# Kernel tuning notes

Hardware: AMD Instinct MI355X
Metric: run time of the kernel (lower is better)

## Reference

```python
import jax, jax.numpy as jnp
import numpy as np

B, C, HS, WS = 4, 256, 64, 64
E, NH, TOPK, MLP = 256, 8, 512, 1024
HD = E // NH
CHUNK = 16   # chunk size over random-query subset for L1 cdist
EPS = 1e-5


def setup_inputs() -> dict:
    key = jax.random.key(0)
    ks = jax.random.split(key, 8)
    s = 0.02
    return {
        "query_source": jax.random.normal(ks[0], (B, C, HS, WS), jnp.float32),
        "context": jax.random.normal(ks[1], (B, C, HS, WS), jnp.float32),
        "rand_token_ind": jax.random.randint(ks[2], (B, TOPK), 0, HS * WS),
        "in_proj_w": jax.random.normal(ks[3], (3 * E, E), jnp.float32) * s,
        "in_proj_b": jnp.zeros((3 * E,), jnp.float32),
        "out_proj_w": jax.random.normal(ks[4], (E, E), jnp.float32) * s,
        "out_proj_b": jnp.zeros((E,), jnp.float32),
        "conv1_w": jax.random.normal(ks[5], (MLP, C), jnp.float32) * s,
        "conv1_b": jnp.zeros((MLP,), jnp.float32),
        "bn1_gamma": jnp.ones((MLP,), jnp.float32),
        "bn1_beta": jnp.zeros((MLP,), jnp.float32),
        "bn1_mean": jnp.zeros((MLP,), jnp.float32),
        "bn1_var": jnp.ones((MLP,), jnp.float32),
        "conv2_w": jax.random.normal(ks[6], (C, MLP), jnp.float32) * s,
        "conv2_b": jnp.zeros((C,), jnp.float32),
        "bn2_gamma": jnp.ones((C,), jnp.float32),
        "bn2_beta": jnp.zeros((C,), jnp.float32),
        "bn2_mean": jnp.zeros((C,), jnp.float32),
        "bn2_var": jnp.ones((C,), jnp.float32),
    }


def _min_l1_dist(K, Qs):
    """min over random-query subset of L1 distances. K:[B,Lkv,D], Qs:[B,tk,D] -> [B,Lkv].
    Chunked scan over tk to avoid materializing [B,Lkv,tk,D]."""
    b, tk, d = Qs.shape
    nc = tk // CHUNK
    Qc = Qs.reshape(b, nc, CHUNK, d).transpose(1, 0, 2, 3)  # [nc,B,CHUNK,D]
    init = jnp.full(K.shape[:2], jnp.inf, K.dtype)

    def step(carry, q):
        dist = jnp.abs(K[:, :, None, :] - q[:, None, :, :]).sum(-1)  # [B,Lkv,CHUNK]
        return jnp.minimum(carry, dist.min(-1)), None

    md, _ = jax.lax.scan(step, init, Qc)
    return md


def _forward(query_source, context, rand_token_ind, in_proj_w, in_proj_b,
             out_proj_w, out_proj_b, conv1_w, conv1_b, bn1_gamma, bn1_beta,
             bn1_mean, bn1_var, conv2_w, conv2_b, bn2_gamma, bn2_beta,
             bn2_mean, bn2_var):
    b, c, h, w = query_source.shape
    q_tok = query_source.reshape(b, c, -1).transpose(0, 2, 1)   # [B,Lq,E]
    kv_tok = context.reshape(b, c, -1).transpose(0, 2, 1)       # [B,Lkv,E]

    # --- dist_to_random_Q_selection (top_k < Lkv) ---
    Qs = jnp.take_along_axis(q_tok, rand_token_ind[:, :, None], axis=1)  # [B,tk,E]
    md = _min_l1_dist(kv_tok, Qs)                                        # [B,Lkv]
    idx = jnp.argsort(md, axis=1)[:, :TOPK]                              # smallest, sorted
    k_sel = jnp.take_along_axis(kv_tok, idx[:, :, None], axis=1)         # [B,TOPK,E]
    v_sel = k_sel                                                        # keys==values==context

    # --- nn.MultiheadAttention (eval, batch_first) ---
    wq, wk, wv = in_proj_w[:E], in_proj_w[E:2 * E], in_proj_w[2 * E:]
    bq, bk, bv = in_proj_b[:E], in_proj_b[E:2 * E], in_proj_b[2 * E:]
    q = (q_tok @ wq.T + bq).reshape(b, -1, NH, HD)
    k = (k_sel @ wk.T + bk).reshape(b, TOPK, NH, HD)
    v = (v_sel @ wv.T + bv).reshape(b, TOPK, NH, HD)
    scores = jnp.einsum('bqhd,bkhd->bhqk', q, k) / jnp.sqrt(jnp.float32(HD))
    attn = jax.nn.softmax(scores, axis=-1)
    ctx = jnp.einsum('bhqk,bkhd->bqhd', attn, v).reshape(b, -1, E)
    out = ctx @ out_proj_w.T + out_proj_b                               # [B,Lq,E]
    attn_out = out.transpose(0, 2, 1).reshape(b, c, h, w)

    # --- residual conv MLP (1x1 convs, batchnorm eval) ---
    def conv1x1(x, wgt, bias):
        return jnp.einsum('bchw,oc->bohw', x, wgt) + bias[None, :, None, None]

    def bn(x, g, bt, m, v_):
        inv = g / jnp.sqrt(v_ + EPS)
        return x * inv[None, :, None, None] + (bt - m * inv)[None, :, None, None]

    hdn = jax.nn.relu(bn(conv1x1(attn_out, conv1_w, conv1_b),
                         bn1_gamma, bn1_beta, bn1_mean, bn1_var))
    y = bn(conv1x1(hdn, conv2_w, conv2_b), bn2_gamma, bn2_beta, bn2_mean, bn2_var)
    return attn_out + y


def reference(query_source, context, rand_token_ind, in_proj_w, in_proj_b,
              out_proj_w, out_proj_b, conv1_w, conv1_b, bn1_gamma, bn1_beta,
              bn1_mean, bn1_var, conv2_w, conv2_b, bn2_gamma, bn2_beta,
              bn2_mean, bn2_var):
    return _forward(query_source, context, rand_token_ind, in_proj_w, in_proj_b,
                    out_proj_w, out_proj_b, conv1_w, conv1_b, bn1_gamma, bn1_beta,
                    bn1_mean, bn1_var, conv2_w, conv2_b, bn2_gamma, bn2_beta,
                    bn2_mean, bn2_var)
```

## Files before the change

kernel.cpp:

```cpp
#include <hip/hip_runtime.h>
#include <math.h>

#define B_ 4
#define C_ 256
#define L_ 4096
#define E_ 256
#define NH_ 8
#define HD_ 32
#define TOPK_ 512
#define MLP_ 1024
#define EPS_ 1e-5f

typedef __attribute__((ext_vector_type(4))) float f32x4;
typedef __attribute__((ext_vector_type(8))) short short8;
typedef __attribute__((ext_vector_type(2))) unsigned int u32x2;
typedef __attribute__((ext_vector_type(4))) unsigned int u32x4;

__device__ __forceinline__ unsigned short f2bf(float x) {
  unsigned u = __float_as_uint(x);
  return (unsigned short)((u + 0x7FFFu + ((u >> 16) & 1)) >> 16);
}
__device__ __forceinline__ float bf2f(unsigned short h) { return __uint_as_float((unsigned)h << 16); }

__device__ __forceinline__ float dpp_red16(float s) {
  s += __int_as_float(__builtin_amdgcn_update_dpp(0, __float_as_int(s), 0x121, 0xF, 0xF, false));
  s += __int_as_float(__builtin_amdgcn_update_dpp(0, __float_as_int(s), 0x122, 0xF, 0xF, false));
  s += __int_as_float(__builtin_amdgcn_update_dpp(0, __float_as_int(s), 0x124, 0xF, 0xF, false));
  s += __int_as_float(__builtin_amdgcn_update_dpp(0, __float_as_int(s), 0x128, 0xF, 0xF, false));
  return s;
}

template <int WRITE_BF>
__global__ __launch_bounds__(256) void k_transpose(const float* __restrict__ in, float* __restrict__ out,
                                                   unsigned short* __restrict__ outbf) {
  __shared__ float tile[32][33];
  int b = blockIdx.z;
  int l0 = blockIdx.x * 32, c0 = blockIdx.y * 32;
  const float* ib = in + (long)b * C_ * L_;
  float* ob = out + (long)b * L_ * C_;
  int tx = threadIdx.x, ty = threadIdx.y;
#pragma unroll
  for (int i = ty; i < 32; i += 8) tile[i][tx] = ib[(long)(c0 + i) * L_ + l0 + tx];
  __syncthreads();
#pragma unroll
  for (int i = ty; i < 32; i += 8) {
    float v = tile[tx][i];
    long off = (long)(l0 + i) * C_ + c0 + tx;
    ob[off] = v;
    if (WRITE_BF) outbf[(long)b * L_ * C_ + off] = f2bf(v);
  }
}

__device__ __forceinline__ void conv_bf8(const float* __restrict__ W, unsigned short* __restrict__ D, int blk) {
  int i = (blk * 256 + threadIdx.x) * 8;
  float4 x = *(const float4*)(W + i);
  float4 y = *(const float4*)(W + i + 4);
  u32x4 w;
  w.x = (unsigned)f2bf(x.x) | ((unsigned)f2bf(x.y) << 16);
  w.y = (unsigned)f2bf(x.z) | ((unsigned)f2bf(x.w) << 16);
  w.z = (unsigned)f2bf(y.x) | ((unsigned)f2bf(y.y) << 16);
  w.w = (unsigned)f2bf(y.z) | ((unsigned)f2bf(y.w) << 16);
  *(u32x4*)(D + i) = w;
}

__global__ __launch_bounds__(256) void k_prep(const float* __restrict__ ipw, const float* __restrict__ opw,
                                              const float* __restrict__ c1w, const float* __restrict__ c2w,
                                              unsigned short* __restrict__ wq_bf, unsigned short* __restrict__ wkv_bf,
                                              unsigned short* __restrict__ c1w_bf, unsigned short* __restrict__ c2w_bf,
                                              unsigned short* __restrict__ opw_d, unsigned* __restrict__ md) {
  int bx = blockIdx.x;
  if (bx < 32) {
    conv_bf8(ipw, wq_bf, bx);
  } else if (bx < 96) {
    conv_bf8(ipw + 65536, wkv_bf, bx - 32);
  } else if (bx < 224) {
    conv_bf8(c1w, c1w_bf, bx - 96);
  } else if (bx < 352) {
    conv_bf8(c2w, c2w_bf, bx - 224);
  } else if (bx < 416) {
    int i = ((bx - 352) * 256 + threadIdx.x) * 4;
    int k = i & 255;
    int n = i >> 8;
    float4 x = *(const float4*)(opw + i);
    unsigned short h0 = f2bf(x.x), h1 = f2bf(x.y), h2 = f2bf(x.z), h3 = f2bf(x.w);
    unsigned short l0 = f2bf(x.x - bf2f(h0)), l1 = f2bf(x.y - bf2f(h1));
    unsigned short l2 = f2bf(x.z - bf2f(h2)), l3 = f2bf(x.w - bf2f(h3));
    u32x2 hv, lv;
    hv.x = (unsigned)h0 | ((unsigned)h1 << 16); hv.y = (unsigned)h2 | ((unsigned)h3 << 16);
    lv.x = (unsigned)l0 | ((unsigned)l1 << 16); lv.y = (unsigned)l2 | ((unsigned)l3 << 16);
    unsigned short* dst = opw_d + (long)n * 512 + (k >> 5) * 64 + (k & 31);
    *(u32x2*)dst = hv;
    *(u32x2*)(dst + 32) = lv;
  } else {
    md[(bx - 416) * 256 + threadIdx.x] = 0x7f800000u;
  }
}

__global__ __launch_bounds__(256) void k_gather_f32(const float* __restrict__ src, const int* __restrict__ ind,
                                                    float* __restrict__ dst, int nrows) {
  int gr = blockIdx.x * 4 + (threadIdx.x >> 6);
  int b = gr / nrows, r = gr % nrows;
  int c = (threadIdx.x & 63) * 4;
  int idx = ind[b * nrows + r];
  *(float4*)(dst + ((long)b * nrows + r) * C_ + c) = *(const float4*)(src + ((long)b * L_ + idx) * C_ + c);
}

__global__ __launch_bounds__(256) void k_gather_bf(const float* __restrict__ src, const int* __restrict__ ind,
                                                   unsigned short* __restrict__ dst, int nrows) {
  int gr = blockIdx.x * 4 + (threadIdx.x >> 6);
  int b = gr / nrows, r = gr % nrows;
  int c = (threadIdx.x & 63) * 4;
  int idx = ind[b * nrows + r];
  float4 x = *(const float4*)(src + ((long)b * L_ + idx) * C_ + c);
  u32x2 w;
  w.x = (unsigned)f2bf(x.x) | ((unsigned)f2bf(x.y) << 16);
  w.y = (unsigned)f2bf(x.z) | ((unsigned)f2bf(x.w) << 16);
  *(u32x2*)(dst + ((long)b * nrows + r) * C_ + c) = w;
}

__global__ __launch_bounds__(256) void k_dist(const float* __restrict__ Kt, const float* __restrict__ Qs,
                                              unsigned* __restrict__ mdbits) {
  __shared__ float Kl[16 * 256];
  __shared__ unsigned mdl[64];
  const int b = blockIdx.y, tb = blockIdx.x, qz = blockIdx.z;
  const int tid = threadIdx.x;
  const int cg = tid & 15, qslot = tid >> 4;
  f32x4 Q[4][4];
  {
    const float* qbase = Qs + ((long)b * TOPK_ + qz * 64 + qslot) * C_ + cg * 4;
#pragma unroll
    for (int r = 0; r < 4; r++)
#pragma unroll
      for (int i = 0; i < 4; i++)
        Q[r][i] = *(volatile const f32x4*)(qbase + (long)r * 16 * C_ + i * 64);
  }
  if (tid < 64) mdl[tid] = 0x7f800000u;
  for (int ck = 0; ck < 4; ck++) {
    __syncthreads();
    {
      const float4* src = (const float4*)(Kt + ((long)b * L_ + tb * 64 + ck * 16) * C_);
      float4* dst = (float4*)Kl;
#pragma unroll
      for (int j = 0; j < 4; j++) dst[tid + j * 256] = src[tid + j * 256];
    }
    __syncthreads();
    for (int t = 0; t < 16; t++) {
      const float* kp = &Kl[t * 256 + cg * 4];
      float4 k0 = *(const float4*)kp;
      float4 k1 = *(const float4*)(kp + 64);
      float4 k2 = *(const float4*)(kp + 128);
      float4 k3 = *(const float4*)(kp + 192);
      float d0, d1, d2, d3;
#define DIST_R(r, dst_)                                                                                   \
  dst_ = (((fabsf(k0.x - Q[r][0].x) + fabsf(k0.y - Q[r][0].y)) +                                          \
           (fabsf(k0.z - Q[r][0].z) + fabsf(k0.w - Q[r][0].w))) +                                         \
          ((fabsf(k1.x - Q[r][1].x) + fabsf(k1.y - Q[r][1].y)) +                                          \
           (fabsf(k1.z - Q[r][1].z) + fabsf(k1.w - Q[r][1].w)))) +                                        \
         (((fabsf(k2.x - Q[r][2].x) + fabsf(k2.y - Q[r][2].y)) +                                          \
           (fabsf(k2.z - Q[r][2].z) + fabsf(k2.w - Q[r][2].w))) +                                         \
          ((fabsf(k3.x - Q[r][3].x) + fabsf(k3.y - Q[r][3].y)) +                                          \
           (fabsf(k3.z - Q[r][3].z) + fabsf(k3.w - Q[r][3].w))))
      DIST_R(0, d0);
      DIST_R(1, d1);
      DIST_R(2, d2);
      DIST_R(3, d3);
#undef DIST_R
      d0 = dpp_red16(d0);
      d1 = dpp_red16(d1);
      d2 = dpp_red16(d2);
      d3 = dpp_red16(d3);
      float mn = fminf(fminf(d0, d1), fminf(d2, d3));
      mn = fminf(mn, __int_as_float(__builtin_amdgcn_ds_swizzle(__float_as_int(mn), 0x401F)));
      if ((tid & 31) == 0) atomicMin(&mdl[ck * 16 + t], __float_as_uint(mn));
    }
  }
  __syncthreads();
  if (tid < 64) atomicMin(&mdbits[(long)b * L_ + tb * 64 + tid], mdl[tid]);
}

__global__ __launch_bounds__(1024) void k_sort(const unsigned* __restrict__ mdb, unsigned* __restrict__ idxsel) {
  __shared__ unsigned long long s[4096];
  const int b = blockIdx.x, tid = threadIdx.x;
  for (int i = tid; i < 4096; i += 1024)
    s[i] = (((unsigned long long)mdb[b * L_ + i]) << 32) | (unsigned)i;
  __syncthreads();
  for (int k = 2; k <= 4096; k <<= 1)
    for (int j = k >> 1; j > 0; j >>= 1) {
      for (int i = tid; i < 4096; i += 1024) {
        int ixj = i ^ j;
        if (ixj > i) {
          bool up = ((i & k) == 0);
          unsigned long long a = s[i], c = s[ixj];
          if ((a > c) == up) { s[i] = c; s[ixj] = a; }
        }
      }
      __syncthreads();
    }
  for (int i = tid; i < TOPK_; i += 1024) idxsel[b * TOPK_ + i] = (unsigned)(s[i] & 0xFFFFFFFFu);
}

template <int BN, int MODE>
__global__ __launch_bounds__(256) void k_gemm_s(
    const unsigned short* __restrict__ A, const unsigned short* __restrict__ Bm, int K, int N, float cscale,
    const float* __restrict__ bias, const float* __restrict__ g, const float* __restrict__ be,
    const float* __restrict__ mu, const float* __restrict__ va, const float* __restrict__ Xres,
    float* __restrict__ Cf, unsigned short* __restrict__ Cb, unsigned short* __restrict__ Caux) {
  constexpr int NWN = (BN == 128) ? 2 : 1;
  constexpr int WR = (NWN == 2) ? 64 : 32;
  constexpr int MG = WR / 16, NG = 4;
  __shared__ __align__(16) unsigned short As[128 * 64];
  __shared__ __align__(16) unsigned short Bs[BN * 64];
  const int tid = threadIdx.x;
  const int wid = tid >> 6, lane = tid & 63, lr = lane & 15, lg = lane >> 4;
  const int wm = wid / NWN, wn = wid % NWN;
  const int row0 = wm * WR, col0 = wn * 64;
  char* AsB = (char*)As;
  char* BsB = (char*)Bs;
  f32x4 acc[MG][NG];
#pragma unroll
  for (int m = 0; m < MG; m++)
#pragma unroll
    for (int n = 0; n < NG; n++) acc[m][n] = (f32x4){0.f, 0.f, 0.f, 0.f};

  for (int k0 = 0; k0 < K; k0 += 64) {
    if (k0) __syncthreads();
    {
      int r = tid >> 1, h = tid & 1;
      const unsigned short* p = A + (long)(blockIdx.y * 128 + r) * K + k0 + h * 32;
#pragma unroll
      for (int j = 0; j < 4; j++) {
        u32x4 w = *(const u32x4*)(p + j * 8);
        int c = h * 4 + j;
        *(u32x4*)(AsB + r * 128 + ((c ^ (r & 7)) << 4)) = w;
      }
    }
    if (BN == 128) {
      int r = tid >> 1, h = tid & 1;
      const unsigned short* p = Bm + (long)(blockIdx.x * 128 + r) * K + k0 + h * 32;
#pragma unroll
      for (int j = 0; j < 4; j++) {
        u32x4 w = *(const u32x4*)(p + j * 8);
        int c = h * 4 + j;
        *(u32x4*)(BsB + r * 128 + ((c ^ (r & 7)) << 4)) = w;
      }
    } else {
      int r = tid >> 2, qp = tid & 3;
      const unsigned short* p = Bm + (long)(blockIdx.x * 64 + r) * K + k0 + qp * 16;
#pragma unroll
      for (int j = 0; j < 2; j++) {
        u32x4 w = *(const u32x4*)(p + j * 8);
        int c = qp * 2 + j;
        *(u32x4*)(BsB + r * 128 + ((c ^ (r & 7)) << 4)) = w;
      }
    }
    __syncthreads();
    short8 a0[MG], a1[MG], b0[NG], b1[NG];
#pragma unroll
    for (int m = 0; m < MG; m++) {
      int rr = row0 + m * 16 + lr;
      a0[m] = *(const short8*)(AsB + rr * 128 + (((0 + lg) ^ (rr & 7)) << 4));
      a1[m] = *(const short8*)(AsB + rr * 128 + (((4 + lg) ^ (rr & 7)) << 4));
    }
#pragma unroll
    for (int n = 0; n < NG; n++) {
      int rr = col0 + n * 16 + lr;
      b0[n] = *(const short8*)(BsB + rr * 128 + (((0 + lg) ^ (rr & 7)) << 4));
      b1[n] = *(const short8*)(BsB + rr * 128 + (((4 + lg) ^ (rr & 7)) << 4));
    }
#pragma unroll
    for (int m = 0; m < MG; m++)
#pragma unroll
      for (int n = 0; n < NG; n++)
        acc[m][n] = __builtin_amdgcn_mfma_f32_16x16x32_bf16(a0[m], b0[n], acc[m][n], 0, 0, 0);
#pragma unroll
    for (int m = 0; m < MG; m++)
#pragma unroll
      for (int n = 0; n < NG; n++)
        acc[m][n] = __builtin_amdgcn_mfma_f32_16x16x32_bf16(a1[m], b1[n], acc[m][n], 0, 0, 0);
  }
  const int mbase = blockIdx.y * 128 + row0 + lg * 4;
  const int nbase = blockIdx.x * BN + col0;
#pragma unroll
  for (int n = 0; n < NG; n++) {
    int nn = nbase + n * 16 + lr;
    float bb = bias[nn];
    float inv = 0.f, sh = 0.f;
    if (MODE == 3 || MODE == 5) {
      inv = g[nn] / sqrtf(va[nn] + EPS_);
      sh = be[nn] - mu[nn] * inv;
    }
#pragma unroll
    for (int m = 0; m < MG; m++) {
#pragma unroll
      for (int r = 0; r < 4; r++) {
        int mm = mbase + m * 16 + r;
        float v = acc[m][n][r] + bb;
        if (MODE == 0) {
          Cb[(long)mm * N + nn] = f2bf(v * cscale);
        } else if (MODE == 1) {
          if (nn < 256) {
            Cb[(long)mm * 256 + nn] = f2bf(v);
          } else {
            int bi = mm >> 9, t = mm & 511;
            Caux[((long)bi * 256 + (nn - 256)) * 512 + t] = f2bf(v);
          }
        } else if (MODE == 3) {
          v = v * inv + sh;
          v = fmaxf(v, 0.f);
          Cb[(long)mm * N + nn] = f2bf(v);
        } else if (MODE == 5) {
          v = v * inv + sh + Xres[(long)mm * 256 + nn];
          int bi = mm >> 12, l = mm & 4095;
          Cf[(long)bi * (C_ * L_) + (long)nn * L_ + l] = v;
        }
      }
    }
  }
}

__global__ __launch_bounds__(256) void k_gemm_d(const unsigned short* __restrict__ A,
                                                const unsigned short* __restrict__ Bd, int K,
                                                const float* __restrict__ bias, float* __restrict__ Cf,
                                                unsigned short* __restrict__ Cb) {
  constexpr int MG = 2, NG = 4;
  __shared__ __align__(16) unsigned short As[128 * 64];
  __shared__ __align__(16) unsigned short Bs[64 * 64];
  const int tid = threadIdx.x;
  const int wid = tid >> 6, lane = tid & 63, lr = lane & 15, lg = lane >> 4;
  const int row0 = wid * 32;
  char* AsB = (char*)As;
  char* BsB = (char*)Bs;
  f32x4 acc[MG][NG];
#pragma unroll
  for (int m = 0; m < MG; m++)
#pragma unroll
    for (int n = 0; n < NG; n++) acc[m][n] = (f32x4){0.f, 0.f, 0.f, 0.f};

  for (int kb = 0; kb < K; kb += 32) {
    if (kb) __syncthreads();
    {
      int r = tid >> 1, h = tid & 1;
      const unsigned short* p = A + (long)(blockIdx.y * 128 + r) * (2 * K) + kb * 2 + h * 32;
#pragma unroll
      for (int j = 0; j < 4; j++) {
        u32x4 w = *(const u32x4*)(p + j * 8);
        int c = h * 4 + j;
        *(u32x4*)(AsB + r * 128 + ((c ^ (r & 7)) << 4)) = w;
      }
    }
    {
      int r = tid >> 2, qp = tid & 3;
      const unsigned short* p = Bd + (long)(blockIdx.x * 64 + r) * (2 * K) + kb * 2 + qp * 16;
#pragma unroll
      for (int j = 0; j < 2; j++) {
        u32x4 w = *(const u32x4*)(p + j * 8);
        int c = qp * 2 + j;
        *(u32x4*)(BsB + r * 128 + ((c ^ (r & 7)) << 4)) = w;
      }
    }
    __syncthreads();
    short8 a0[MG], a1[MG], b0[NG], b1[NG];
#pragma unroll
    for (int m = 0; m < MG; m++) {
      int rr = row0 + m * 16 + lr;
      a0[m] = *(const short8*)(AsB + rr * 128 + (((0 + lg) ^ (rr & 7)) << 4));
      a1[m] = *(const short8*)(AsB + rr * 128 + (((4 + lg) ^ (rr & 7)) << 4));
    }
#pragma unroll
    for (int n = 0; n < NG; n++) {
      int rr = n * 16 + lr;
      b0[n] = *(const short8*)(BsB + rr * 128 + (((0 + lg) ^ (rr & 7)) << 4));
      b1[n] = *(const short8*)(BsB + rr * 128 + (((4 + lg) ^ (rr & 7)) << 4));
    }
#pragma unroll
    for (int m = 0; m < MG; m++)
#pragma unroll
      for (int n = 0; n < NG; n++)
        acc[m][n] = __builtin_amdgcn_mfma_f32_16x16x32_bf16(a0[m], b0[n], acc[m][n], 0, 0, 0);
#pragma unroll
    for (int m = 0; m < MG; m++)
#pragma unroll
      for (int n = 0; n < NG; n++)
        acc[m][n] = __builtin_amdgcn_mfma_f32_16x16x32_bf16(a1[m], b0[n], acc[m][n], 0, 0, 0);
#pragma unroll
    for (int m = 0; m < MG; m++)
#pragma unroll
      for (int n = 0; n < NG; n++)
        acc[m][n] = __builtin_amdgcn_mfma_f32_16x16x32_bf16(a0[m], b1[n], acc[m][n], 0, 0, 0);
  }
  const int mbase = blockIdx.y * 128 + row0 + lg * 4;
  const int nbase = blockIdx.x * 64;
#pragma unroll
  for (int n = 0; n < NG; n++) {
    int nn = nbase + n * 16 + lr;
    float bb = bias[nn];
#pragma unroll
    for (int m = 0; m < MG; m++) {
#pragma unroll
      for (int r = 0; r < 4; r++) {
        int mm = mbase + m * 16 + r;
        float v = acc[m][n][r] + bb;
        Cf[(long)mm * 256 + nn] = v;
        Cb[(long)mm * 256 + nn] = f2bf(v);
      }
    }
  }
}

__global__ __launch_bounds__(256) void k_attn_mfma(const unsigned short* __restrict__ qbf,
                                                   const unsigned short* __restrict__ kvk,
                                                   const unsigned short* __restrict__ vt,
                                                   unsigned short* __restrict__ ctxd) {
  __shared__ __align__(16) unsigned short PT[4 * 1024];
  const int tid = threadIdx.x, wid = tid >> 6, lane = tid & 63, lr = lane & 15, lg = lane >> 4;
  const int b = blockIdx.z, h = blockIdx.y;
  const int q0 = blockIdx.x * 64 + wid * 16;
  char* pt = (char*)(PT + wid * 1024);
  short8 qf = *(const short8*)(qbf + ((long)(b * L_ + q0 + lr)) * E_ + h * HD_ + lg * 8);
  f32x4 o0 = (f32x4){0.f, 0.f, 0.f, 0.f}, o1 = (f32x4){0.f, 0.f, 0.f, 0.f};
  float lsum = 0.f;
  for (int t0 = 0; t0 < TOPK_; t0 += 64) {
    f32x4 sc[4];
#pragma unroll
    for (int f = 0; f < 4; f++) {
      short8 kf = *(const short8*)(kvk + ((long)(b * TOPK_ + t0 + f * 16 + lr)) * E_ + h * HD_ + lg * 8);
      f32x4 z = (f32x4){0.f, 0.f, 0.f, 0.f};
      sc[f] = __builtin_amdgcn_mfma_f32_16x16x32_bf16(kf, qf, z, 0, 0, 0);
    }
    float csum = 0.f;
#pragma unroll
    for (int f = 0; f < 4; f++) {
      float e0 = __expf(sc[f][0]), e1 = __expf(sc[f][1]), e2 = __expf(sc[f][2]), e3 = __expf(sc[f][3]);
      csum += (e0 + e1) + (e2 + e3);
      u32x2 w;
      w.x = (unsigned)f2bf(e0) | ((unsigned)f2bf(e1) << 16);
      w.y = (unsigned)f2bf(e2) | ((unsigned)f2bf(e3) << 16);
      *(u32x2*)(pt + lr * 128 + ((((f * 2 + (lg >> 1)) ^ (lr & 7))) << 4) + (lg & 1) * 8) = w;
    }
    csum += __shfl_xor(csum, 16);
    csum += __shfl_xor(csum, 32);
    lsum += csum;
#pragma unroll
    for (int ks = 0; ks < 2; ks++) {
      short8 pf = *(const short8*)(pt + lr * 128 + (((ks * 4 + lg) ^ (lr & 7)) << 4));
      {
        short8 vf = *(const short8*)(vt + ((long)(b * 256 + h * HD_ + 0 + lr)) * 512 + t0 + ks * 32 + lg * 8);
        o0 = __builtin_amdgcn_mfma_f32_16x16x32_bf16(pf, vf, o0, 0, 0, 0);
      }
      {
        short8 vf = *(const short8*)(vt + ((long)(b * 256 + h * HD_ + 16 + lr)) * 512 + t0 + ks * 32 + lg * 8);
        o1 = __builtin_amdgcn_mfma_f32_16x16x32_bf16(pf, vf, o1, 0, 0, 0);
      }
    }
  }
#pragma unroll
  for (int r = 0; r < 4; r++) {
    float li = 1.0f / __shfl(lsum, lg * 4 + r);
    long base = ((long)(b * L_ + q0 + lg * 4 + r)) * 512 + h * 64;
    float v0 = o0[r] * li, v1 = o1[r] * li;
    unsigned short h0 = f2bf(v0), h1 = f2bf(v1);
    ctxd[base + lr] = h0;
    ctxd[base + 32 + lr] = f2bf(v0 - bf2f(h0));
    ctxd[base + 16 + lr] = h1;
    ctxd[base + 48 + lr] = f2bf(v1 - bf2f(h1));
  }
}

extern "C" void kernel_launch(void* const* d_in, const int* in_sizes, int n_in, void* d_out, int out_size, void* d_ws,
                              size_t ws_size, hipStream_t stream) {
  (void)in_sizes; (void)n_in; (void)out_size; (void)ws_size;
  const float* qs_in = (const float*)d_in[0];
  const float* ctx_in = (const float*)d_in[1];
  const int* rind = (const int*)d_in[2];
  const float* ipw = (const float*)d_in[3];
  const float* ipb = (const float*)d_in[4];
  const float* opw = (const float*)d_in[5];
  const float* opb = (const float*)d_in[6];
  const float* c1w = (const float*)d_in[7];
  const float* c1b = (const float*)d_in[8];
  const float* g1 = (const float*)d_in[9];
  const float* b1 = (const float*)d_in[10];
  const float* mu1 = (const float*)d_in[11];
  const float* v1 = (const float*)d_in[12];
  const float* c2w = (const float*)d_in[13];
  const float* c2b = (const float*)d_in[14];
  const float* g2 = (const float*)d_in[15];
  const float* b2 = (const float*)d_in[16];
  const float* mu2 = (const float*)d_in[17];
  const float* v2 = (const float*)d_in[18];
  float* out = (float*)d_out;
  float* ws = (float*)d_ws;

  float* Qt = ws;
  unsigned short* ctxd = (unsigned short*)ws;
  float* Kt = ws + 4194304;
  float* X = ws + 4194304;
  unsigned short* Qt_bf = (unsigned short*)(ws + 8388608);
  unsigned short* X_bf = (unsigned short*)(ws + 8388608);
  float* Qsbuf = ws + 10485760;
  unsigned* md = (unsigned*)(ws + 11010048);
  unsigned* idxsel = (unsigned*)(ws + 11026432);
  unsigned short* ksel_bf = (unsigned short*)(ws + 11272192);
  unsigned short* q_bf = (unsigned short*)(ws + 11534336);
  unsigned short* kv_k = (unsigned short*)(ws + 13631488);
  unsigned short* v_t = (unsigned short*)(ws + 13893632);
  unsigned short* H = (unsigned short*)(ws + 10485760);
  unsigned short* wq_bf = (unsigned short*)(ws + 18874368);
  unsigned short* wkv_bf = (unsigned short*)(ws + 18907136);
  unsigned short* c1w_bf = (unsigned short*)(ws + 18972672);
  unsigned short* c2w_bf = (unsigned short*)(ws + 19103744);
  unsigned short* opw_d = (unsigned short*)(ws + 19234816);

  const float qscale = 0.17677669529663687f;

  k_prep<<<480, 256, 0, stream>>>(ipw, opw, c1w, c2w, wq_bf, wkv_bf, c1w_bf, c2w_bf, opw_d, md);

  dim3 tb(32, 8);
  k_transpose<1><<<dim3(128, 8, 4), tb, 0, stream>>>(qs_in, Qt, Qt_bf);
  k_transpose<0><<<dim3(128, 8, 4), tb, 0, stream>>>(ctx_in, Kt, nullptr);
  k_gather_f32<<<512, 256, 0, stream>>>(Qt, rind, Qsbuf, TOPK_);
  k_dist<<<dim3(64, 4, 8), 256, 0, stream>>>(Kt, Qsbuf, md);
  k_sort<<<4, 1024, 0, stream>>>(md, idxsel);
  k_gather_bf<<<512, 256, 0, stream>>>(Kt, (const int*)idxsel, ksel_bf, TOPK_);

  k_gemm_s<64, 0><<<dim3(4, 128), 256, 0, stream>>>(Qt_bf, wq_bf, 256, 256, qscale, ipb, nullptr, nullptr, nullptr,
                                                    nullptr, nullptr, nullptr, q_bf, nullptr);
  k_gemm_s<64, 1><<<dim3(8, 16), 256, 0, stream>>>(ksel_bf, wkv_bf, 256, 512, 1.f, ipb + 256, nullptr, nullptr,
                                                   nullptr, nullptr, nullptr, nullptr, kv_k, v_t);
  k_attn_mfma<<<dim3(64, NH_, B_), 256, 0, stream>>>(q_bf, kv_k, v_t, ctxd);
  k_gemm_d<<<dim3(4, 128), 256, 0, stream>>>(ctxd, opw_d, 256, opb, X, X_bf);
  k_gemm_s<128, 3><<<dim3(8, 128), 256, 0, stream>>>(X_bf, c1w_bf, 256, 1024, 1.f, c1b, g1, b1, mu1, v1, nullptr,
                                                     nullptr, H, nullptr);
  k_gemm_s<64, 5><<<dim3(4, 128), 256, 0, stream>>>(H, c2w_bf, 1024, 256, 1.f, c2b, g2, b2, mu2, v2, X, out,
                                                    nullptr, nullptr);
}
```

Baseline: 335.8 us.

## Replace bitonic top-k sort with radix select and merge setup kernels

The full 4096-element bitonic sort per batch is replaced by a 32-pass bitwise radix select that finds the 512th smallest threshold via ballot counts, then emits indices below it and breaks ties by lowest index. Weight prep and both input transposes are merged into one launch to cut launch overhead, and k_dist is marked to avoid AGPR allocation. Output index order changes from sorted to arbitrary, which is fine only if downstream attention is order-invariant over keys. The serial tie-break loop on one thread could be slow if many ties exist.

```diff
diff --git a/kernel.cpp b/kernel.cpp
--- a/kernel.cpp
+++ b/kernel.cpp
@@ -11,6 +11,12 @@
 #define MLP_ 1024
 #define EPS_ 1e-5f
 
+#if __has_attribute(amdgpu_agpr_alloc)
+#define NO_AGPR __attribute__((amdgpu_agpr_alloc(0)))
+#else
+#define NO_AGPR
+#endif
+
 typedef __attribute__((ext_vector_type(4))) float f32x4;
 typedef __attribute__((ext_vector_type(8))) short short8;
 typedef __attribute__((ext_vector_type(2))) unsigned int u32x2;
@@ -30,29 +36,9 @@
   return s;
 }
 
-template <int WRITE_BF>
-__global__ __launch_bounds__(256) void k_transpose(const float* __restrict__ in, float* __restrict__ out,
-                                                   unsigned short* __restrict__ outbf) {
-  __shared__ float tile[32][33];
-  int b = blockIdx.z;
-  int l0 = blockIdx.x * 32, c0 = blockIdx.y * 32;
-  const float* ib = in + (long)b * C_ * L_;
-  float* ob = out + (long)b * L_ * C_;
-  int tx = threadIdx.x, ty = threadIdx.y;
-#pragma unroll
-  for (int i = ty; i < 32; i += 8) tile[i][tx] = ib[(long)(c0 + i) * L_ + l0 + tx];
-  __syncthreads();
-#pragma unroll
-  for (int i = ty; i < 32; i += 8) {
-    float v = tile[tx][i];
-    long off = (long)(l0 + i) * C_ + c0 + tx;
-    ob[off] = v;
-    if (WRITE_BF) outbf[(long)b * L_ * C_ + off] = f2bf(v);
-  }
-}
-
-__device__ __forceinline__ void conv_bf8(const float* __restrict__ W, unsigned short* __restrict__ D, int blk) {
-  int i = (blk * 256 + threadIdx.x) * 8;
+__device__ __forceinline__ void conv_bf8(const float* __restrict__ W, unsigned short* __restrict__ D, int blk,
+                                         int tid) {
+  int i = (blk * 256 + tid) * 8;
   float4 x = *(const float4*)(W + i);
   float4 y = *(const float4*)(W + i + 4);
   u32x4 w;
@@ -63,36 +49,69 @@
   *(u32x4*)(D + i) = w;
 }
 
-__global__ __launch_bounds__(256) void k_prep(const float* __restrict__ ipw, const float* __restrict__ opw,
-                                              const float* __restrict__ c1w, const float* __restrict__ c2w,
-                                              unsigned short* __restrict__ wq_bf, unsigned short* __restrict__ wkv_bf,
-                                              unsigned short* __restrict__ c1w_bf, unsigned short* __restrict__ c2w_bf,
-                                              unsigned short* __restrict__ opw_d, unsigned* __restrict__ md) {
-  int bx = blockIdx.x;
-  if (bx < 32) {
-    conv_bf8(ipw, wq_bf, bx);
-  } else if (bx < 96) {
-    conv_bf8(ipw + 65536, wkv_bf, bx - 32);
-  } else if (bx < 224) {
-    conv_bf8(c1w, c1w_bf, bx - 96);
-  } else if (bx < 352) {
-    conv_bf8(c2w, c2w_bf, bx - 224);
-  } else if (bx < 416) {
-    int i = ((bx - 352) * 256 + threadIdx.x) * 4;
-    int k = i & 255;
-    int n = i >> 8;
-    float4 x = *(const float4*)(opw + i);
-    unsigned short h0 = f2bf(x.x), h1 = f2bf(x.y), h2 = f2bf(x.z), h3 = f2bf(x.w);
-    unsigned short l0 = f2bf(x.x - bf2f(h0)), l1 = f2bf(x.y - bf2f(h1));
-    unsigned short l2 = f2bf(x.z - bf2f(h2)), l3 = f2bf(x.w - bf2f(h3));
-    u32x2 hv, lv;
-    hv.x = (unsigned)h0 | ((unsigned)h1 << 16); hv.y = (unsigned)h2 | ((unsigned)h3 << 16);
-    lv.x = (unsigned)l0 | ((unsigned)l1 << 16); lv.y = (unsigned)l2 | ((unsigned)l3 << 16);
-    unsigned short* dst = opw_d + (long)n * 512 + (k >> 5) * 64 + (k & 31);
-    *(u32x2*)dst = hv;
-    *(u32x2*)(dst + 32) = lv;
+__global__ __launch_bounds__(256) void k_setup(const float* __restrict__ ipw, const float* __restrict__ opw,
+                                               const float* __restrict__ c1w, const float* __restrict__ c2w,
+                                               const float* __restrict__ qs_in, const float* __restrict__ ctx_in,
+                                               unsigned short* __restrict__ wq_bf, unsigned short* __restrict__ wkv_bf,
+                                               unsigned short* __restrict__ c1w_bf, unsigned short* __restrict__ c2w_bf,
+                                               unsigned short* __restrict__ opw_d, unsigned* __restrict__ md,
+                                               float* __restrict__ Qt, unsigned short* __restrict__ Qt_bf,
+                                               float* __restrict__ Kt) {
+  __shared__ float tile[32][33];
+  const int bx = blockIdx.x;
+  const int tid = threadIdx.x;
+  if (bx < 480) {
+    if (bx < 32) {
+      conv_bf8(ipw, wq_bf, bx, tid);
+    } else if (bx < 96) {
+      conv_bf8(ipw + 65536, wkv_bf, bx - 32, tid);
+    } else if (bx < 224) {
+      conv_bf8(c1w, c1w_bf, bx - 96, tid);
+    } else if (bx < 352) {
+      conv_bf8(c2w, c2w_bf, bx - 224, tid);
+    } else if (bx < 416) {
+      int i = ((bx - 352) * 256 + tid) * 4;
+      int k = i & 255;
+      int n = i >> 8;
+      float4 x = *(const float4*)(opw + i);
+      unsigned short h0 = f2bf(x.x), h1 = f2bf(x.y), h2 = f2bf(x.z), h3 = f2bf(x.w);
+      unsigned short l0 = f2bf(x.x - bf2f(h0)), l1 = f2bf(x.y - bf2f(h1));
+      unsigned short l2 = f2bf(x.z - bf2f(h2)), l3 = f2bf(x.w - bf2f(h3));
+      u32x2 hv, lv;
+      hv.x = (unsigned)h0 | ((unsigned)h1 << 16); hv.y = (unsigned)h2 | ((unsigned)h3 << 16);
+      lv.x = (unsigned)l0 | ((unsigned)l1 << 16); lv.y = (unsigned)l2 | ((unsigned)l3 << 16);
+      unsigned short* dst = opw_d + (long)n * 512 + (k >> 5) * 64 + (k & 31);
+      *(u32x2*)dst = hv;
+      *(u32x2*)(dst + 32) = lv;
+    } else {
+      md[(bx - 416) * 256 + tid] = 0x7f800000u;
+    }
+    return;
+  }
+  int tb = bx - 480;
+  const float* in;
+  float* out;
+  unsigned short* outbf;
+  int wbf;
+  if (tb < 4096) {
+    in = qs_in; out = Qt; outbf = Qt_bf; wbf = 1;
   } else {
-    md[(bx - 416) * 256 + threadIdx.x] = 0x7f800000u;
+    tb -= 4096; in = ctx_in; out = Kt; outbf = nullptr; wbf = 0;
+  }
+  const int x = tb & 127, y = (tb >> 7) & 7, b = tb >> 10;
+  const int l0 = x * 32, c0 = y * 32;
+  const int tx = tid & 31, ty = tid >> 5;
+  const float* ib = in + (long)b * C_ * L_;
+  float* ob = out + (long)b * L_ * C_;
+#pragma unroll
+  for (int i = ty; i < 32; i += 8) tile[i][tx] = ib[(long)(c0 + i) * L_ + l0 + tx];
+  __syncthreads();
+#pragma unroll
+  for (int i = ty; i < 32; i += 8) {
+    float v = tile[tx][i];
+    long off = (long)(l0 + i) * C_ + c0 + tx;
+    ob[off] = v;
+    if (wbf) outbf[(long)b * L_ * C_ + off] = f2bf(v);
   }
 }
 
@@ -118,8 +137,8 @@
   *(u32x2*)(dst + ((long)b * nrows + r) * C_ + c) = w;
 }
 
-__global__ __launch_bounds__(256) void k_dist(const float* __restrict__ Kt, const float* __restrict__ Qs,
-                                              unsigned* __restrict__ mdbits) {
+__global__ __launch_bounds__(256) NO_AGPR void k_dist(const float* __restrict__ Kt, const float* __restrict__ Qs,
+                                                      unsigned* __restrict__ mdbits) {
   __shared__ float Kl[16 * 256];
   __shared__ unsigned mdl[64];
   const int b = blockIdx.y, tb = blockIdx.x, qz = blockIdx.z;
@@ -178,25 +197,59 @@
   if (tid < 64) atomicMin(&mdbits[(long)b * L_ + tb * 64 + tid], mdl[tid]);
 }
 
-__global__ __launch_bounds__(1024) void k_sort(const unsigned* __restrict__ mdb, unsigned* __restrict__ idxsel) {
-  __shared__ unsigned long long s[4096];
+__global__ __launch_bounds__(1024) void k_select(const unsigned* __restrict__ mdb, unsigned* __restrict__ idxsel) {
+  __shared__ unsigned vals[4096];
+  __shared__ unsigned cnts[32];
+  __shared__ unsigned out_n, tie_n;
+  __shared__ unsigned short ties[1024];
   const int b = blockIdx.x, tid = threadIdx.x;
-  for (int i = tid; i < 4096; i += 1024)
-    s[i] = (((unsigned long long)mdb[b * L_ + i]) << 32) | (unsigned)i;
+  const int lane = tid & 63;
+#pragma unroll
+  for (int s = 0; s < 4; s++) vals[tid + s * 1024] = mdb[b * 4096 + tid + s * 1024];
+  if (tid < 32) cnts[tid] = 0;
+  if (tid == 0) { out_n = 0; tie_n = 0; }
   __syncthreads();
-  for (int k = 2; k <= 4096; k <<= 1)
-    for (int j = k >> 1; j > 0; j >>= 1) {
-      for (int i = tid; i < 4096; i += 1024) {
-        int ixj = i ^ j;
-        if (ixj > i) {
-          bool up = ((i & k) == 0);
-          unsigned long long a = s[i], c = s[ixj];
-          if ((a > c) == up) { s[i] = c; s[ixj] = a; }
-        }
-      }
-      __syncthreads();
-    }
-  for (int i = tid; i < TOPK_; i += 1024) idxsel[b * TOPK_ + i] = (unsigned)(s[i] & 0xFFFFFFFFu);
+  unsigned cur = 0;
+  for (int bit = 31; bit >= 0; --bit) {
+    unsigned cand = cur | (1u << bit);
+    int c = 0;
+#pragma unroll
+    for (int s = 0; s < 4; s++) {
+      unsigned long long bal = __ballot(vals[tid + s * 1024] < cand);
+      c += __popcll(bal);
+    }
+    if (lane == 0) atomicAdd(&cnts[bit], (unsigned)c);
+    __syncthreads();
+    if (cnts[bit] < 512u) cur = cand;
+  }
+  const unsigned M = cur;
+#pragma unroll
+  for (int s = 0; s < 4; s++) {
+    int i = tid + s * 1024;
+    unsigned v = vals[i];
+    if (v < M) {
+      unsigned p = atomicAdd(&out_n, 1u);
+      idxsel[b * TOPK_ + p] = (unsigned)i;
+    } else if (v == M) {
+      unsigned t = atomicAdd(&tie_n, 1u);
+      if (t < 1024u) ties[t] = (unsigned short)i;
+    }
+  }
+  __syncthreads();
+  if (tid == 0) {
+    int n1 = (int)out_n;
+    int nt = (int)tie_n; if (nt > 1024) nt = 1024;
+    int need = 512 - n1; if (need > nt) need = nt;
+    for (int j = 0; j < need; j++) {
+      int bi = 1 << 30, best = -1;
+      for (int t = 0; t < nt; t++) {
+        int ix = ties[t];
+        if (ix < bi) { bi = ix; best = t; }
+      }
+      ties[best] = 0xFFFF;
+      idxsel[b * TOPK_ + n1 + j] = (unsigned)bi;
+    }
+  }
 }
 
 template <int BN, int MODE>
@@ -513,14 +566,11 @@
 
   const float qscale = 0.17677669529663687f;
 
-  k_prep<<<480, 256, 0, stream>>>(ipw, opw, c1w, c2w, wq_bf, wkv_bf, c1w_bf, c2w_bf, opw_d, md);
-
-  dim3 tb(32, 8);
-  k_transpose<1><<<dim3(128, 8, 4), tb, 0, stream>>>(qs_in, Qt, Qt_bf);
-  k_transpose<0><<<dim3(128, 8, 4), tb, 0, stream>>>(ctx_in, Kt, nullptr);
+  k_setup<<<8672, 256, 0, stream>>>(ipw, opw, c1w, c2w, qs_in, ctx_in, wq_bf, wkv_bf, c1w_bf, c2w_bf, opw_d, md, Qt,
+                                    Qt_bf, Kt);
   k_gather_f32<<<512, 256, 0, stream>>>(Qt, rind, Qsbuf, TOPK_);
   k_dist<<<dim3(64, 4, 8), 256, 0, stream>>>(Kt, Qsbuf, md);
-  k_sort<<<4, 1024, 0, stream>>>(md, idxsel);
+  k_select<<<4, 1024, 0, stream>>>(md, idxsel);
   k_gather_bf<<<512, 256, 0, stream>>>(Kt, (const int*)idxsel, ksel_bf, TOPK_);
 
   k_gemm_s<64, 0><<<dim3(4, 128), 256, 0, stream>>>(Qt_bf, wq_bf, 256, 256, qscale, ipb, nullptr, nullptr, nullptr,
```

Measured after the change: 283.4 us. 15.6% less time.
